# Kernel optimization log

Measured on AMD Instinct MI355X. Metric: run time of the kernel, lower is better.

The kernel has to match this reference:

```python
import jax, jax.numpy as jnp
import numpy as np

VAR0, VAR1 = 0.1, 0.2
THRESHOLD = 0.35
NEGPOS_RATIO = 7
LOW_GT_THRESH = 0.2  # match() filters GT whose best prior IoU < 0.2


def setup_inputs() -> dict:
    key = jax.random.key(0)
    ks = jax.random.split(key, 8)
    B, P, G = 16, 43008, 128
    loc_data = jax.random.normal(ks[0], (B, P, 4), jnp.float32)
    conf_data = jax.random.normal(ks[1], (B, P, 2), jnp.float32)
    landm_data = jax.random.normal(ks[2], (B, P, 10), jnp.float32)
    # priors in cxcywh form, positive sizes
    pc = jax.random.uniform(ks[3], (P, 2), jnp.float32)
    pwh = jax.random.uniform(ks[4], (P, 2), jnp.float32, minval=0.02, maxval=0.32)
    priors = jnp.concatenate([pc, pwh], axis=1)
    # targets: valid xyxy boxes + 10 landmark coords + label (face=1)
    ctr = jax.random.uniform(ks[5], (B, G, 2), jnp.float32, minval=0.2, maxval=0.8)
    wh = jax.random.uniform(ks[6], (B, G, 2), jnp.float32, minval=0.05, maxval=0.3)
    boxes = jnp.concatenate([ctr - wh / 2, ctr + wh / 2], axis=-1)
    landms = jax.random.uniform(ks[7], (B, G, 10), jnp.float32)
    labels = jnp.ones((B, G, 1), jnp.float32)
    targets = jnp.concatenate([boxes, landms, labels], axis=-1)
    return {"loc_data": loc_data, "conf_data": conf_data, "landm_data": landm_data,
            "priors": priors, "targets": targets}


def point_form(priors):
    return jnp.concatenate([priors[:, :2] - priors[:, 2:] / 2,
                            priors[:, :2] + priors[:, 2:] / 2], axis=1)


def jaccard(a, b):  # a: [G,4] xyxy, b: [P,4] xyxy -> [G,P]
    lt = jnp.maximum(a[:, None, :2], b[None, :, :2])
    rb = jnp.minimum(a[:, None, 2:], b[None, :, 2:])
    wh = jnp.clip(rb - lt, 0.0)
    inter = wh[..., 0] * wh[..., 1]
    area_a = (a[:, 2] - a[:, 0]) * (a[:, 3] - a[:, 1])
    area_b = (b[:, 2] - b[:, 0]) * (b[:, 3] - b[:, 1])
    return inter / (area_a[:, None] + area_b[None, :] - inter)


def encode(matched, priors):  # matched xyxy [P,4], priors cxcywh [P,4]
    g_cxcy = (matched[:, :2] + matched[:, 2:]) / 2 - priors[:, :2]
    g_cxcy = g_cxcy / (VAR0 * priors[:, 2:])
    g_wh = jnp.log((matched[:, 2:] - matched[:, :2]) / priors[:, 2:]) / VAR1
    return jnp.concatenate([g_cxcy, g_wh], axis=1)


def encode_landm(matched, priors):  # matched [P,10], priors [P,4]
    m = matched.reshape(-1, 5, 2)
    g = (m - priors[:, None, :2]) / (VAR0 * priors[:, None, 2:])
    return g.reshape(-1, 10)


def match_one(truths, labels, landms, priors):
    G = truths.shape[0]
    overlaps = jaccard(truths, point_form(priors))  # [G, P]
    best_prior_overlap = overlaps.max(axis=1)       # [G]
    best_prior_idx = overlaps.argmax(axis=1)        # [G]
    valid = best_prior_overlap >= LOW_GT_THRESH
    any_valid = jnp.any(valid)
    best_truth_overlap = overlaps.max(axis=0)       # [P]
    best_truth_idx = overlaps.argmax(axis=0)        # [P]
    # index_fill_(0, best_prior_idx_filter, 2): ensure each valid GT keeps its best prior
    fill_val = jnp.where(valid, 2.0, best_truth_overlap[best_prior_idx])
    best_truth_overlap = best_truth_overlap.at[best_prior_idx].set(fill_val)
    # best_truth_idx[best_prior_idx[j]] = j for all j
    best_truth_idx = best_truth_idx.at[best_prior_idx].set(jnp.arange(G))
    matches = truths[best_truth_idx]                       # [P,4]
    conf = labels[best_truth_idx].astype(jnp.int32)        # [P]
    conf = jnp.where(best_truth_overlap < THRESHOLD, 0, conf)
    conf = jnp.where(any_valid, conf, 0)  # no valid GT -> all background
    loc = encode(matches, priors)
    landm = encode_landm(landms[best_truth_idx], priors)
    return loc, conf, landm


def smooth_l1(x):
    ax = jnp.abs(x)
    return jnp.where(ax < 1.0, 0.5 * ax * ax, ax - 0.5)


def reference(loc_data, conf_data, landm_data, priors, targets):
    truths = targets[..., :4]
    landms = targets[..., 4:14]
    labels = targets[..., 14]
    loc_t, conf_t, landm_t = jax.vmap(
        lambda t, l, lm: match_one(t, l, lm, priors))(truths, labels, landms)

    # landmark loss over positives
    pos1 = conf_t > 0
    N1 = jnp.maximum(pos1.sum().astype(jnp.float32), 1.0)
    loss_landm = jnp.sum(smooth_l1(landm_data - landm_t) * pos1[..., None])

    # localization loss over positives
    pos = conf_t != 0
    num_pos = pos.sum(axis=1, keepdims=True)  # [B,1]
    loss_l = jnp.sum(smooth_l1(loc_data - loc_t) * pos[..., None])

    # hard negative mining on per-prior CE loss
    lse = jax.scipy.special.logsumexp(conf_data, axis=-1)  # [B,P]
    gathered = jnp.take_along_axis(conf_data, conf_t[..., None], axis=-1)[..., 0]
    ce_all = lse - gathered                                # [B,P] per-prior CE
    mine = jnp.where(pos, 0.0, ce_all)
    loss_idx = jnp.argsort(-mine, axis=1)
    idx_rank = jnp.argsort(loss_idx, axis=1)
    num_neg = jnp.clip(NEGPOS_RATIO * num_pos, None, pos.shape[1] - 1)
    neg = idx_rank < num_neg
    sel = pos | neg
    loss_c = jnp.sum(jnp.where(sel, ce_all, 0.0))

    N = jnp.maximum(num_pos.sum().astype(jnp.float32), 1.0)
    return loss_l / N, loss_c / N, loss_landm / N1
```

## Files before the change

### kernel.cpp

```cpp
#include <hip/hip_runtime.h>
#include <stdint.h>


#define GC 8
#define PPI 2
#define NCELL 1024

__device__ __forceinline__ float sl1(float x) {
  float a = fabsf(x);
  return a < 1.f ? 0.5f * a * a : a - 0.5f;
}

__device__ __forceinline__ double dwave(double v) {
#pragma unroll
  for (int o = 32; o; o >>= 1) v += __shfl_down(v, o);
  return v;
}

__device__ __forceinline__ int cellOf(float4 pr) {
  int cx = (int)(pr.x * 16.f); cx = cx < 0 ? 0 : (cx > 15 ? 15 : cx);
  int cy = (int)(pr.y * 16.f); cy = cy < 0 ? 0 : (cy > 15 ? 15 : cy);
  return ((cy * 16 + cx) << 2) | ((pr.z > 0.17f) ? 2 : 0) |
         ((pr.w > 0.17f) ? 1 : 0);
}

__device__ __forceinline__ unsigned bsufscan(unsigned x, unsigned* S,
                                             unsigned* wt, int tid) {
  int lane = tid & 63, wid = tid >> 6;
  unsigned v = x;
#pragma unroll
  for (int o = 1; o < 64; o <<= 1) {
    unsigned u = __shfl_down(v, o);
    if (lane + o < 64) v += u;
  }
  if (lane == 0) wt[wid] = v;
  __syncthreads();
  if (wid == 0) {
    unsigned tv = (lane < 16) ? wt[lane] : 0;
#pragma unroll
    for (int o = 1; o < 16; o <<= 1) {
      unsigned u = __shfl_down(tv, o);
      if (lane + o < 64) tv += u;
    }
    if (lane < 16) wt[lane] = tv;
  }
  __syncthreads();
  unsigned Sv = v + ((wid < 15) ? wt[wid + 1] : 0u);
  S[tid] = Sv;
  __syncthreads();
  return Sv;
}

__global__ __launch_bounds__(256) void k_hist(const float* __restrict__ priors,
                                              unsigned* __restrict__ cellh,
                                              int P) {
  int p = blockIdx.x * 256 + threadIdx.x;
  if (p < P) {
    float4 pr = ((const float4*)priors)[p];
    atomicAdd(&cellh[cellOf(pr)], 1u);
  }
}

__global__ __launch_bounds__(1024) void k_scan(const unsigned* __restrict__ cellh,
                                               unsigned* __restrict__ cellcur) {
  int tid = threadIdx.x;
  __shared__ unsigned s[NCELL];
  unsigned v = cellh[tid];
  s[tid] = v;
  __syncthreads();
  for (int off = 1; off < NCELL; off <<= 1) {
    unsigned a = (tid >= off) ? s[tid - off] : 0u;
    __syncthreads();
    s[tid] += a;
    __syncthreads();
  }
  cellcur[tid] = s[tid] - v;
}

__global__ __launch_bounds__(256) void k_scatter(
    const float* __restrict__ priors, unsigned* __restrict__ cellcur,
    float4* __restrict__ spr, unsigned* __restrict__ sid,
    unsigned* __restrict__ inv, int P) {
  int p = blockIdx.x * 256 + threadIdx.x;
  if (p < P) {
    float4 pr = ((const float4*)priors)[p];
    unsigned pos = atomicAdd(&cellcur[cellOf(pr)], 1u);
    spr[pos] = pr;
    sid[pos] = (unsigned)p;
    inv[p] = pos;
  }
}

__global__ __launch_bounds__(64) void k_wgm(
    const float4* __restrict__ spr, const float* __restrict__ targets,
    uint4* __restrict__ gmask, unsigned* __restrict__ zbase, int zwords,
    int G, int NRW, int B, int P) {
  int run = blockIdx.x, lane = threadIdx.x;
  for (int i = run * 64 + lane; i < zwords; i += NRW * 64) zbase[i] = 0u;

  int p = run * 64 + lane;
  float x1 = 1e30f, y1 = 1e30f, x2 = -1e30f, y2 = -1e30f;
  if (p < P) {
    float4 pr = spr[p];
    x1 = pr.x - pr.z * 0.5f; y1 = pr.y - pr.w * 0.5f;
    x2 = pr.x + pr.z * 0.5f; y2 = pr.y + pr.w * 0.5f;
  }
#pragma unroll
  for (int o = 32; o; o >>= 1) {
    x1 = fminf(x1, __shfl_down(x1, o));
    y1 = fminf(y1, __shfl_down(y1, o));
    x2 = fmaxf(x2, __shfl_down(x2, o));
    y2 = fmaxf(y2, __shfl_down(y2, o));
  }
  x1 = __shfl(x1, 0); y1 = __shfl(y1, 0);
  x2 = __shfl(x2, 0); y2 = __shfl(y2, 0);

  for (int b = 0; b < B; ++b) {
    const float* t0 = targets + ((size_t)b * G + lane) * 15;
    const float* t1 = targets + ((size_t)b * G + lane + 64) * 15;
    bool o0 = (t0[0] < x2) && (x1 < t0[2]) && (t0[1] < y2) && (y1 < t0[3]);
    bool o1 = (t1[0] < x2) && (x1 < t1[2]) && (t1[1] < y2) && (y1 < t1[3]);
    unsigned long long b0 = __ballot(o0);
    unsigned long long b1 = __ballot(o1);
    if (lane == 0)
      gmask[(size_t)b * NRW + run] =
          make_uint4((unsigned)b0, (unsigned)(b0 >> 32), (unsigned)b1,
                     (unsigned)(b1 >> 32));
  }
}

__global__ __launch_bounds__(256) void k_mm(
    const float4* __restrict__ spr, const unsigned* __restrict__ sid,
    const uint4* __restrict__ gmask, const float* __restrict__ conf,
    const float* __restrict__ targets, const float* __restrict__ loc,
    const float* __restrict__ lm, uint2* __restrict__ ovti,
    unsigned long long* __restrict__ bp, float* __restrict__ mine,
    unsigned* __restrict__ ghist, double* __restrict__ pll,
    double* __restrict__ pllm, double* __restrict__ plc,
    double* __restrict__ msum, int* __restrict__ pnp, int P, int G, int NIOU,
    int PTI, int NGC, int PC, int NRW) {
  int tid = threadIdx.x;
  __shared__ char smem[16384];
  __shared__ float4 sgt[128];
  __shared__ float sga[128];

  if ((int)blockIdx.x < NIOU) {
    float* st = (float*)smem;
    double* rs = (double*)(smem + 7680);
    int* ri = (int*)(smem + 7808);
    unsigned* hist = (unsigned*)(smem + 8192);
    unsigned* smaskw = (unsigned*)(smem + 12288);
    int b = blockIdx.x / PTI, tile = blockIdx.x % PTI;
    int base = tile * (256 * PPI);
    for (int i = tid; i < G * 15; i += 256)
      st[i] = targets[(size_t)b * G * 15 + i];
    for (int g = tid; g < G; g += 256) {
      const float* t = targets + ((size_t)b * G + g) * 15;
      float x1 = t[0], y1 = t[1], x2 = t[2], y2 = t[3];
      sgt[g] = make_float4(x1, y1, x2, y2);
      sga[g] = (x2 - x1) * (y2 - y1);
    }
    for (int i = tid; i < 1024; i += 256) hist[i] = 0;
    if (tid < 8 * 4)
      smaskw[tid] =
          ((const unsigned*)(gmask + (size_t)b * NRW + tile * (4 * PPI)))[tid];
    __syncthreads();

    float px1[PPI], py1[PPI], px2[PPI], py2[PPI], pa[PPI];
    float bi[PPI], sb[PPI];
    int bidx[PPI];
#pragma unroll
    for (int k = 0; k < PPI; ++k) {
      int p = base + tid + k * 256;
      int pl = p < P ? p : P - 1;
      float4 pr = spr[pl];
      px1[k] = pr.x - pr.z * 0.5f; py1[k] = pr.y - pr.w * 0.5f;
      px2[k] = pr.x + pr.z * 0.5f; py2[k] = pr.y + pr.w * 0.5f;
      pa[k] = pr.z * pr.w;
      bi[k] = 0.f; sb[k] = 1.f; bidx[k] = 0;
    }

#define IOU_UPD(GG)                                                        \
  {                                                                        \
    float iw = fminf(T.z, px2[k]) - fmaxf(T.x, px1[k]);                    \
    float ih = fminf(T.w, py2[k]) - fmaxf(T.y, py1[k]);                    \
    float inter = fmaxf(iw, 0.f) * ih;                                     \
    float S = A + pa[k];                                                   \
    if (inter * sb[k] > bi[k] * S) { bi[k] = inter; sb[k] = S; bidx[k] = (GG); } \
  }
#pragma unroll
    for (int k = 0; k < PPI; ++k) {
      int runl = k * 4 + (tid >> 6);
      unsigned mw0 = smaskw[runl * 4 + 0], mw1 = smaskw[runl * 4 + 1];
      unsigned mw2 = smaskw[runl * 4 + 2], mw3 = smaskw[runl * 4 + 3];
      unsigned long long m0 =
          ((unsigned long long)(unsigned)__builtin_amdgcn_readfirstlane(
               (int)mw1)
           << 32) |
          (unsigned)__builtin_amdgcn_readfirstlane((int)mw0);
      unsigned long long m1 =
          ((unsigned long long)(unsigned)__builtin_amdgcn_readfirstlane(
               (int)mw3)
           << 32) |
          (unsigned)__builtin_amdgcn_readfirstlane((int)mw2);
      while (m0) {
        int g = __builtin_ctzll(m0);
        m0 &= m0 - 1;
        float4 T = sgt[g];
        float A = sga[g];
        IOU_UPD(g)
      }
      while (m1) {
        int g = 64 + __builtin_ctzll(m1);
        m1 &= m1 - 1;
        float4 T = sgt[g];
        float A = sga[g];
        IOU_UPD(g)
      }
    }
#undef IOU_UPD

    double ll = 0, llm = 0, lc = 0, ms = 0;
    int np = 0;
#pragma unroll
    for (int k = 0; k < PPI; ++k) {
      int p = base + tid + k * 256;
      if (p < P) {
        size_t idxs = (size_t)b * P + p;
        float ov = bi[k] / (sb[k] - bi[k]);
        int ti = bidx[k];
        ovti[idxs] = make_uint2(__float_as_uint(ov), (unsigned)ti);
        bool pos = ov >= 0.35f;
        unsigned op = sid[p];
        size_t idxo = (size_t)b * P + op;
        float2 c = ((const float2*)conf)[idxo];
        float mx = fmaxf(c.x, c.y);
        float dd = fabsf(c.x - c.y);
        float lse = mx + logf(1.f + expf(-dd));
        float ce = lse - (pos ? c.y : c.x);
        float mv = pos ? 0.f : ce;
        mine[idxs] = mv;
        atomicAdd(&hist[__float_as_uint(mv) >> 21], 1u);
        ms += (double)mv;
        if (pos) {
          np++;
          lc += (double)ce;
          float4 pr = spr[p];
          const float* t = st + ti * 15;
          float rz = 1.f / pr.z, rw = 1.f / pr.w;
          float rdx = 10.f * rz, rdy = 10.f * rw;
          float gx = ((t[0] + t[2]) * 0.5f - pr.x) * rdx;
          float gy = ((t[1] + t[3]) * 0.5f - pr.y) * rdy;
          float gw = logf((t[2] - t[0]) * rz) * 5.0f;
          float gh = logf((t[3] - t[1]) * rw) * 5.0f;
          float4 ld = ((const float4*)loc)[idxo];
          ll += (double)(sl1(ld.x - gx) + sl1(ld.y - gy) + sl1(ld.z - gw) +
                         sl1(ld.w - gh));
          const float2* lmd = (const float2*)lm + idxo * 5;
          float s = 0.f;
#pragma unroll
          for (int j = 0; j < 5; ++j) {
            float2 lv = lmd[j];
            float ex = (t[4 + 2 * j] - pr.x) * rdx;
            float ey = (t[5 + 2 * j] - pr.y) * rdy;
            s += sl1(lv.x - ex) + sl1(lv.y - ey);
          }
          llm += (double)s;
        }
      }
    }

    ll = dwave(ll); llm = dwave(llm); lc = dwave(lc); ms = dwave(ms);
#pragma unroll
    for (int o = 32; o; o >>= 1) np += __shfl_down(np, o);
    int lane = tid & 63, wid = tid >> 6;
    if (lane == 0) {
      rs[wid] = ll; rs[4 + wid] = llm; rs[8 + wid] = lc; rs[12 + wid] = ms;
      ri[wid] = np;
    }
    __syncthreads();
    if (tid == 0) {
      pll[blockIdx.x] = rs[0] + rs[1] + rs[2] + rs[3];
      pllm[blockIdx.x] = rs[4] + rs[5] + rs[6] + rs[7];
      plc[blockIdx.x] = rs[8] + rs[9] + rs[10] + rs[11];
      msum[blockIdx.x] = rs[12] + rs[13] + rs[14] + rs[15];
      pnp[blockIdx.x] = ri[0] + ri[1] + ri[2] + ri[3];
    }
    for (int i = tid; i < 1024; i += 256) {
      unsigned c = hist[i];
      if (c) atomicAdd(&ghist[b * 1024 + i], c);
    }
  } else {
    unsigned long long* sred = (unsigned long long*)smem;
    unsigned char* bm = (unsigned char*)sga;
    int bc = blockIdx.x - NIOU;
    int pc = bc % PC;
    int gcb = (bc / PC) % NGC;
    int b = bc / (PC * NGC);
    int g0 = gcb * GC;

    int chunk = (P + PC - 1) / PC;
    int ps = pc * chunk;
    int pe = ps + chunk; if (pe > P) pe = P;
    int count = pe - ps;
    int nrun = (count + 63) >> 6;

    if (tid < GC) {
      int g = g0 + tid;
      float4 v = make_float4(0.f, 0.f, 0.f, 0.f);
      if (g < G) {
        const float* t = targets + ((size_t)b * G + g) * 15;
        v = make_float4(t[0], t[1], t[2], t[3]);
      }
      sgt[tid] = v;
    }
    if (tid < nrun) {
      uint4 m = gmask[(size_t)b * NRW + (ps >> 6) + tid];
      unsigned word = (g0 & 64) ? ((g0 & 32) ? m.w : m.z)
                                : ((g0 & 32) ? m.y : m.x);
      bm[tid] = (unsigned char)((word >> (g0 & 31)) & 0xffu);
    }
    __syncthreads();

    float gx1[GC], gy1[GC], gx2[GC], gy2[GC], ga[GC];
#pragma unroll
    for (int j = 0; j < GC; ++j) {
      float4 T = sgt[j];
      gx1[j] = T.x; gy1[j] = T.y; gx2[j] = T.z; gy2[j] = T.w;
      ga[j] = (T.z - T.x) * (T.w - T.y);
    }

    float bi[GC], sb[GC];
    unsigned bpp[GC];
#pragma unroll
    for (int j = 0; j < GC; ++j) { bi[j] = 0.f; sb[j] = 1.f; bpp[j] = 0xFFFFFFFFu; }

#define BP_BODY(X1, Y1, X2, Y2, AR, PP)                                     \
  {                                                                         \
    float iw = fminf(gx2[j], X2) - fmaxf(gx1[j], X1);                       \
    float ih = fminf(gy2[j], Y2) - fmaxf(gy1[j], Y1);                       \
    float inter = fmaxf(iw, 0.f) * ih;                                      \
    float S = ga[j] + AR;                                                   \
    if (inter * sb[j] > bi[j] * S) { bi[j] = inter; sb[j] = S; bpp[j] = (PP); } \
  }
    for (int i = tid; i < count; i += 1024) {
      int ib = __builtin_amdgcn_readfirstlane(i);
      int rl = ib >> 6;
      int i1 = i + 256, i2 = i + 512, i3 = i + 768;
      int p0 = ps + i;
      int p1 = (i1 < count) ? ps + i1 : p0;
      int p2 = (i2 < count) ? ps + i2 : p0;
      int p3 = (i3 < count) ? ps + i3 : p0;
      unsigned by0 = bm[rl];
      unsigned by1 = bm[(ib + 256 < count) ? rl + 4 : rl];
      unsigned by2 = bm[(ib + 512 < count) ? rl + 8 : rl];
      unsigned by3 = bm[(ib + 768 < count) ? rl + 12 : rl];
      by0 = (unsigned)__builtin_amdgcn_readfirstlane((int)by0);
      by1 = (unsigned)__builtin_amdgcn_readfirstlane((int)by1);
      by2 = (unsigned)__builtin_amdgcn_readfirstlane((int)by2);
      by3 = (unsigned)__builtin_amdgcn_readfirstlane((int)by3);
      float4 q0 = spr[p0];
      float4 q1 = spr[p1];
      float4 q2 = spr[p2];
      float4 q3 = spr[p3];
      unsigned s0 = sid[p0], s1 = sid[p1], s2 = sid[p2], s3 = sid[p3];
      float ax1 = q0.x - q0.z * 0.5f, ay1 = q0.y - q0.w * 0.5f;
      float ax2 = q0.x + q0.z * 0.5f, ay2 = q0.y + q0.w * 0.5f;
      float aa = q0.z * q0.w;
      float bx1 = q1.x - q1.z * 0.5f, by1f = q1.y - q1.w * 0.5f;
      float bx2 = q1.x + q1.z * 0.5f, by2f = q1.y + q1.w * 0.5f;
      float ba = q1.z * q1.w;
      float cx1 = q2.x - q2.z * 0.5f, cy1 = q2.y - q2.w * 0.5f;
      float cx2 = q2.x + q2.z * 0.5f, cy2 = q2.y + q2.w * 0.5f;
      float ca = q2.z * q2.w;
      float dx1 = q3.x - q3.z * 0.5f, dy1 = q3.y - q3.w * 0.5f;
      float dx2 = q3.x + q3.z * 0.5f, dy2 = q3.y + q3.w * 0.5f;
      float da = q3.z * q3.w;
#pragma unroll
      for (int j = 0; j < GC; ++j) {
        if (by0 & (1u << j)) BP_BODY(ax1, ay1, ax2, ay2, aa, s0)
        if (by1 & (1u << j)) BP_BODY(bx1, by1f, bx2, by2f, ba, s1)
        if (by2 & (1u << j)) BP_BODY(cx1, cy1, cx2, cy2, ca, s2)
        if (by3 & (1u << j)) BP_BODY(dx1, dy1, dx2, dy2, da, s3)
      }
    }
#undef BP_BODY

#pragma unroll
    for (int j = 0; j < GC; ++j) {
      float iou = bi[j] / (sb[j] - bi[j]);
      unsigned long long pk =
          ((unsigned long long)__float_as_uint(iou) << 32) | (unsigned)(~bpp[j]);
      sred[j * 256 + tid] = pk;
    }
    __syncthreads();
    {
      int j = tid >> 5, s = tid & 31;
      unsigned long long m = sred[j * 256 + s];
#pragma unroll
      for (int t = 1; t < 8; ++t) {
        unsigned long long v = sred[j * 256 + s + t * 32];
        if (v > m) m = v;
      }
      __syncthreads();
      sred[j * 256 + s] = m;
    }
    __syncthreads();
    if (tid < GC) {
      unsigned long long m = sred[tid * 256];
      for (int s = 1; s < 32; ++s) {
        unsigned long long v = sred[tid * 256 + s];
        if (v > m) m = v;
      }
      int g = g0 + tid;
      if (g < G) atomicMax(&bp[(size_t)b * G + g], m);
    }
  }
}

__global__ __launch_bounds__(1024) void k_tail2(
    const unsigned long long* __restrict__ bp, const unsigned* __restrict__ inv,
    uint2* __restrict__ ovti, const float* __restrict__ conf,
    const float* __restrict__ loc, const float* __restrict__ lm,
    const float* __restrict__ priors, const float* __restrict__ targets,
    float* __restrict__ mine, unsigned* __restrict__ ghist,
    const int* __restrict__ pnp, const double* __restrict__ msum,
    const double* __restrict__ pll, const double* __restrict__ pllm,
    const double* __restrict__ plc, double* __restrict__ gacc,
    int* __restrict__ gnp, unsigned* __restrict__ done,
    float* __restrict__ out, int P, int G, int PTI, int B) {
  int b = blockIdx.x, tid = threadIdx.x;
  int lane = tid & 63, wid = tid >> 6;
  __shared__ unsigned spp[128];
  __shared__ double rs[16 * 5];
  __shared__ int ris[16];
  __shared__ unsigned S[1024];
  __shared__ unsigned hs[2048];
  __shared__ unsigned wt[16];
  __shared__ double sdel[4];
  __shared__ int sdnp, sav, smode;
  __shared__ long long sk;
  __shared__ double sA, sC, sD;
  __shared__ int snpos;
  __shared__ int st_, sk1_;
  __shared__ unsigned lcnt;
  __shared__ int spf21, sk2;
  __shared__ unsigned stb;
  __shared__ double stie;

  double dll = 0, dllm = 0, dlc = 0, dms = 0;
  int dnp = 0;
  unsigned pp = 0;
  bool valid = false;
  if (tid < G) {
    unsigned long long m = bp[(size_t)b * G + tid];
    pp = (m == 0ull) ? 0u : ~(unsigned)m;
    float val = __uint_as_float((unsigned)(m >> 32));
    spp[tid] = pp;
    valid = val >= 0.2f;
  }
  int av = __syncthreads_or((tid < G && valid) ? 1 : 0);
  bool win = false;
  if (tid < G) {
    win = true;
    for (int g2 = tid + 1; g2 < G; ++g2)
      if (spp[g2] == pp) { win = false; break; }
  }
  if (win) {
    size_t idx = (size_t)b * P + pp;
    unsigned sp = inv[pp];
    size_t idxs = (size_t)b * P + sp;
    uint2 ot = ovti[idxs];
    float ov_o = __uint_as_float(ot.x);
    int ti_o = (int)ot.y;
    float ov_n = valid ? 2.0f : ov_o;
    int ti_n = tid;
    bool pos_o = ov_o >= 0.35f, pos_n = ov_n >= 0.35f;

    float2 c = ((const float2*)conf)[idx];
    float mx = fmaxf(c.x, c.y);
    float dd = fabsf(c.x - c.y);
    float lse = mx + logf(1.f + expf(-dd));
    float ce_o = lse - (pos_o ? c.y : c.x);
    float ce_n = lse - (pos_n ? c.y : c.x);
    float mv_o = mine[idxs];
    float mv_n = pos_n ? 0.f : ce_n;
    if (mv_n != mv_o) {
      mine[idxs] = mv_n;
      atomicSub(&ghist[b * 1024 + (__float_as_uint(mv_o) >> 21)], 1u);
      atomicAdd(&ghist[b * 1024 + (__float_as_uint(mv_n) >> 21)], 1u);
    }
    dms = (double)mv_n - (double)mv_o;
    dnp = (pos_n ? 1 : 0) - (pos_o ? 1 : 0);
    dlc = (pos_n ? (double)ce_n : 0.0) - (pos_o ? (double)ce_o : 0.0);

    if (pos_o || pos_n) {
      float4 pr = ((const float4*)priors)[pp];
      float rz = 1.f / pr.z, rw = 1.f / pr.w;
      float rdx = 10.f * rz, rdy = 10.f * rw;
      float4 ld = ((const float4*)loc)[idx];
      const float2* lmd = (const float2*)lm + idx * 5;
      float2 lv[5];
#pragma unroll
      for (int j = 0; j < 5; ++j) lv[j] = lmd[j];
      for (int pass = 0; pass < 2; ++pass) {
        bool act = pass ? pos_n : pos_o;
        int ti = pass ? ti_n : ti_o;
        if (!act) continue;
        const float* t = targets + ((size_t)b * G + ti) * 15;
        float gx = ((t[0] + t[2]) * 0.5f - pr.x) * rdx;
        float gy = ((t[1] + t[3]) * 0.5f - pr.y) * rdy;
        float gw = logf((t[2] - t[0]) * rz) * 5.0f;
        float gh = logf((t[3] - t[1]) * rw) * 5.0f;
        double l = (double)(sl1(ld.x - gx) + sl1(ld.y - gy) +
                            sl1(ld.z - gw) + sl1(ld.w - gh));
        float s = 0.f;
#pragma unroll
        for (int j = 0; j < 5; ++j) {
          float ex = (t[4 + 2 * j] - pr.x) * rdx;
          float ey = (t[5 + 2 * j] - pr.y) * rdy;
          s += sl1(lv[j].x - ex) + sl1(lv[j].y - ey);
        }
        if (pass) { dll += l; dllm += (double)s; }
        else { dll -= l; dllm -= (double)s; }
      }
    }
  }
  dll = dwave(dll); dllm = dwave(dllm); dlc = dwave(dlc); dms = dwave(dms);
#pragma unroll
  for (int o = 32; o; o >>= 1) dnp += __shfl_down(dnp, o);
  if (lane == 0) {
    rs[wid] = dll; rs[16 + wid] = dllm; rs[32 + wid] = dlc; rs[48 + wid] = dms;
    ris[wid] = dnp;
  }
  __syncthreads();
  if (tid == 0) {
    double a = 0, c2 = 0, d2 = 0, m2 = 0;
    int n2 = 0;
    for (int i = 0; i < 16; ++i) {
      a += rs[i]; c2 += rs[16 + i]; d2 += rs[32 + i]; m2 += rs[48 + i];
      n2 += ris[i];
    }
    sdel[0] = a; sdel[1] = c2; sdel[2] = d2; sdel[3] = m2;
    sdnp = n2; sav = av;
  }
  __syncthreads();

  double a = 0, cc = 0, d = 0, ms = 0;
  int n = 0;
  for (int i = tid; i < PTI; i += 1024) {
    int ix = b * PTI + i;
    a += pll[ix]; cc += pllm[ix]; d += plc[ix]; ms += msum[ix]; n += pnp[ix];
  }
  a = dwave(a); cc = dwave(cc); d = dwave(d); ms = dwave(ms);
#pragma unroll
  for (int o = 32; o; o >>= 1) n += __shfl_down(n, o);
  if (lane == 0) {
    rs[wid] = a; rs[16 + wid] = cc; rs[32 + wid] = d; rs[48 + wid] = ms;
    ris[wid] = n;
  }
  __syncthreads();
  double Fv = 0.0;
  if (tid == 0) {
    double A = 0, C = 0, D = 0, MS = 0;
    int npos = 0;
    for (int i = 0; i < 16; ++i) {
      A += rs[i]; C += rs[16 + i]; D += rs[32 + i]; MS += rs[48 + i];
      npos += ris[i];
    }
    A += sdel[0]; C += sdel[1]; D += sdel[2]; MS += sdel[3];
    npos += sdnp;
    if (!sav) { A = 0; C = 0; D = 0; npos = 0; }
    sA = A; sC = C; sD = D; snpos = npos;
    long long k = 7LL * (long long)npos;
    long long cap = P - 1;
    int md = 1;
    if (k <= 0) { Fv = 0.0; md = 0; }
    else if (k >= cap) { Fv = MS; md = 0; }
    smode = md; sk = k;
  }
  __syncthreads();

  if (smode) {
    long long k = sk;
    {
      unsigned x = ghist[b * 1024 + tid];
      unsigned Sv = bsufscan(x, S, wt, tid);
      int cnt_ = __syncthreads_count((long long)Sv >= k);
      int seg = cnt_ - 1;
      if (tid == seg) {
        long long cum = (seg + 1 < 1024) ? (long long)S[seg + 1] : 0;
        st_ = seg;
        sk1_ = (int)(k - cum);
      }
      if (tid == 0) lcnt = 0;
    }
    __syncthreads();
    int t = st_;
    long long k1 = (long long)sk1_;

    const float* mrow = mine + (size_t)b * P;
    float* crow = (float*)(ovti + (size_t)b * P);
    double acc = 0;
    for (int base0 = 0; base0 < P; base0 += 4096) {
#pragma unroll
      for (int j = 0; j < 4; ++j) {
        int p = base0 + tid + j * 1024;
        bool keep = false;
        unsigned bb = 0;
        if (p < P) {
          bb = __float_as_uint(mrow[p]);
          int bin = (int)(bb >> 21);
          if (bin > t) acc += (double)__uint_as_float(bb);
          else keep = (bin == t);
        }
        unsigned long long mk = __ballot(keep);
        int nset = __popcll(mk);
        if (nset) {
          unsigned wbase = 0;
          if (lane == 0) wbase = atomicAdd(&lcnt, (unsigned)nset);
          wbase = __shfl(wbase, 0);
          if (keep) {
            int offi = __popcll(mk & ((1ull << lane) - 1ull));
            crow[wbase + offi] = __uint_as_float(bb);
          }
        }
      }
    }
    acc = dwave(acc);
    if (lane == 0) rs[wid] = acc;
    __syncthreads();
    int nn = (int)lcnt;

    hs[tid] = 0; hs[tid + 1024] = 0;
    __syncthreads();
    for (int i = tid; i < nn; i += 1024) {
      unsigned bb = __float_as_uint(crow[i]);
      atomicAdd(&hs[(bb >> 10) & 2047], 1u);
    }
    __syncthreads();
    {
      unsigned h0 = hs[tid * 2], h1v = hs[tid * 2 + 1];
      unsigned Sv = bsufscan(h0 + h1v, S, wt, tid);
      int cnt_ = __syncthreads_count((long long)Sv >= k1);
      int seg = cnt_ - 1;
      if (tid == seg) {
        long long cum = (seg + 1 < 1024) ? (long long)S[seg + 1] : 0;
        int bin = seg * 2;
        if (cum + h1v >= k1) bin = seg * 2 + 1;
        else cum += h1v;
        spf21 = (t << 11) | bin;
        sk2 = (int)(k1 - cum);
      }
    }
    __syncthreads();
    int pf21 = spf21;

    hs[tid] = 0;
    __syncthreads();
    for (int i = tid; i < nn; i += 1024) {
      unsigned bb = __float_as_uint(crow[i]);
      if ((int)(bb >> 10) == pf21) atomicAdd(&hs[bb & 1023], 1u);
    }
    __syncthreads();
    {
      unsigned Sv = bsufscan(hs[tid], S, wt, tid);
      long long kk = (long long)sk2;
      int cnt_ = __syncthreads_count((long long)Sv >= kk);
      int seg = cnt_ - 1;
      if (tid == seg) {
        long long cum = (seg + 1 < 1024) ? (long long)S[seg + 1] : 0;
        unsigned tb = ((unsigned)pf21 << 10) | (unsigned)seg;
        stb = tb;
        stie = (double)(kk - cum) * (double)__uint_as_float(tb);
      }
    }
    __syncthreads();

    unsigned tb = stb;
    double v = 0.0;
    for (int i = tid; i < nn; i += 1024) {
      unsigned bb = __float_as_uint(crow[i]);
      if (bb > tb) v += (double)__uint_as_float(bb);
    }
    v = dwave(v);
    if (lane == 0) rs[16 + wid] = v;
    __syncthreads();
    if (tid == 0) {
      double hi = 0, vt = 0;
      for (int i = 0; i < 16; ++i) { hi += rs[i]; vt += rs[16 + i]; }
      Fv = hi + vt + stie;
    }
  }

  if (tid == 0) {
    atomicAdd(&gacc[0], sA);
    atomicAdd(&gacc[1], sC);
    atomicAdd(&gacc[2], sD);
    atomicAdd(&gacc[3], Fv);
    atomicAdd(gnp, snpos);
    __threadfence();
    unsigned old = atomicAdd(done, 1u);
    if (old == (unsigned)B - 1) {
      __threadfence();
      double A = atomicAdd(&gacc[0], 0.0);
      double C = atomicAdd(&gacc[1], 0.0);
      double D = atomicAdd(&gacc[2], 0.0);
      double F = atomicAdd(&gacc[3], 0.0);
      int N = atomicAdd(gnp, 0);
      double Nd = N < 1 ? 1.0 : (double)N;
      out[0] = (float)(A / Nd);
      out[1] = (float)((D + F) / Nd);
      out[2] = (float)(C / Nd);
    }
  }
}

extern "C" void kernel_launch(void* const* d_in, const int* in_sizes, int n_in,
                              void* d_out, int out_size, void* d_ws,
                              size_t ws_size, hipStream_t stream) {
  const float* loc = (const float*)d_in[0];
  const float* conf = (const float*)d_in[1];
  const float* lm = (const float*)d_in[2];
  const float* priors = (const float*)d_in[3];
  const float* targets = (const float*)d_in[4];

  int P = in_sizes[3] / 4;
  int B = in_sizes[0] / (4 * P);
  int G = in_sizes[4] / (15 * B);
  int PTI = (P + 256 * PPI - 1) / (256 * PPI);
  int NIOU = B * PTI;
  int NGC = (G + GC - 1) / GC;
  int PC = 8;
  int NBP = B * NGC * PC;
  int NPB = (P + 255) / 256;
  int NRW = (P + 63) / 64;
  int NW = B * NRW;

  char* w = (char*)d_ws;
  size_t off = 0;
  unsigned long long* bp = (unsigned long long*)(w + off);
  off += (size_t)B * G * 8;
  unsigned* ghist = (unsigned*)(w + off);
  off += (size_t)B * 1024 * 4;
  double* gacc = (double*)(w + off);
  off += 4 * 8;
  int* gnp = (int*)(w + off);
  off += 4;
  unsigned* done = (unsigned*)(w + off);
  off += 4;
  size_t clear_bytes = off;
  off = (off + 255) & ~(size_t)255;
  float4* spr = (float4*)(w + off);
  off += (size_t)NRW * 64 * 16;
  unsigned* sid = (unsigned*)(w + off);
  off += (size_t)P * 4;
  unsigned* inv = (unsigned*)(w + off);
  off += (size_t)P * 4;
  uint4* gmask = (uint4*)(w + off);
  off += (size_t)NW * 16;
  unsigned* cellh = (unsigned*)(w + off);
  off += (size_t)NCELL * 4;
  unsigned* cellcur = (unsigned*)(w + off);
  off += (size_t)NCELL * 4;
  off = (off + 255) & ~(size_t)255;
  uint2* ovti = (uint2*)(w + off);
  off += (size_t)B * P * 8;
  float* mine = (float*)(w + off);
  off += (size_t)B * P * 4;
  double* pll = (double*)(w + off);
  off += (size_t)NIOU * 8;
  double* pllm = (double*)(w + off);
  off += (size_t)NIOU * 8;
  double* plc = (double*)(w + off);
  off += (size_t)NIOU * 8;
  double* msum = (double*)(w + off);
  off += (size_t)NIOU * 8;
  int* pnp = (int*)(w + off);
  off += (size_t)NIOU * 4;

  hipMemsetAsync(cellh, 0, (size_t)NCELL * 4, stream);

  k_hist<<<NPB, 256, 0, stream>>>(priors, cellh, P);
  k_scan<<<1, 1024, 0, stream>>>(cellh, cellcur);
  k_scatter<<<NPB, 256, 0, stream>>>(priors, cellcur, spr, sid, inv, P);
  k_wgm<<<NRW, 64, 0, stream>>>(spr, targets, gmask, (unsigned*)w,
                                (int)(clear_bytes / 4), G, NRW, B, P);
  k_mm<<<NIOU + NBP, 256, 0, stream>>>(spr, sid, gmask, conf, targets, loc,
                                       lm, ovti, bp, mine, ghist, pll, pllm,
                                       plc, msum, pnp, P, G, NIOU, PTI, NGC,
                                       PC, NRW);
  k_tail2<<<B, 1024, 0, stream>>>(bp, inv, ovti, conf, loc, lm, priors,
                                  targets, mine, ghist, pnp, msum, pll, pllm,
                                  plc, gacc, gnp, done, (float*)d_out, P, G,
                                  PTI, B);
}
```

Measured before the change: 202.5 us.

## Fuse prior sort prep into one cooperative kernel and raise PPI to four

Replaces the memset plus four small launches (histogram, scan, scatter, window-mask) with one cooperative kernel that uses grid-wide syncs between phases. The per-block scan is rewritten with wave shuffles. PPI is doubled so each IoU block handles more priors, and the mask-load count is adjusted to match. Grid syncs have their own cost, and NPB blocks (168) must all be co-resident for the cooperative launch to succeed. Fewer IoU blocks may also lower parallelism in k_mm.

```diff
diff --git a/kernel.cpp b/kernel.cpp
--- a/kernel.cpp
+++ b/kernel.cpp
@@ -1,9 +1,12 @@
 #include <hip/hip_runtime.h>
+#include <hip/hip_cooperative_groups.h>
 #include <stdint.h>
 
+namespace cg = cooperative_groups;
+
 
 #define GC 8
-#define PPI 2
+#define PPI 4
 #define NCELL 1024
 
 __device__ __forceinline__ float sl1(float x) {
@@ -51,81 +54,92 @@
   return Sv;
 }
 
-__global__ __launch_bounds__(256) void k_hist(const float* __restrict__ priors,
-                                              unsigned* __restrict__ cellh,
-                                              int P) {
-  int p = blockIdx.x * 256 + threadIdx.x;
-  if (p < P) {
-    float4 pr = ((const float4*)priors)[p];
+__global__ __launch_bounds__(256) void k_prep(
+    const float* __restrict__ priors, const float* __restrict__ targets,
+    float4* __restrict__ spr, unsigned* __restrict__ sid,
+    unsigned* __restrict__ inv, uint4* __restrict__ gmask,
+    unsigned* __restrict__ cellh, unsigned* __restrict__ cellcur,
+    unsigned* __restrict__ zbase, int zwords, int P, int G, int NRW, int B) {
+  cg::grid_group grid = cg::this_grid();
+  __shared__ unsigned wsum[4];
+  int tid = threadIdx.x;
+  int gid = blockIdx.x * 256 + tid;
+  int total = gridDim.x * 256;
+
+  for (int i = gid; i < zwords; i += total) zbase[i] = 0u;
+  for (int i = gid; i < NCELL; i += total) cellh[i] = 0u;
+  grid.sync();
+
+  if (gid < P) {
+    float4 pr = ((const float4*)priors)[gid];
     atomicAdd(&cellh[cellOf(pr)], 1u);
   }
-}
-
-__global__ __launch_bounds__(1024) void k_scan(const unsigned* __restrict__ cellh,
-                                               unsigned* __restrict__ cellcur) {
-  int tid = threadIdx.x;
-  __shared__ unsigned s[NCELL];
-  unsigned v = cellh[tid];
-  s[tid] = v;
-  __syncthreads();
-  for (int off = 1; off < NCELL; off <<= 1) {
-    unsigned a = (tid >= off) ? s[tid - off] : 0u;
-    __syncthreads();
-    s[tid] += a;
-    __syncthreads();
-  }
-  cellcur[tid] = s[tid] - v;
-}
-
-__global__ __launch_bounds__(256) void k_scatter(
-    const float* __restrict__ priors, unsigned* __restrict__ cellcur,
-    float4* __restrict__ spr, unsigned* __restrict__ sid,
-    unsigned* __restrict__ inv, int P) {
-  int p = blockIdx.x * 256 + threadIdx.x;
-  if (p < P) {
-    float4 pr = ((const float4*)priors)[p];
+  grid.sync();
+
+  if (blockIdx.x == 0) {
+    int lane = tid & 63, wv = tid >> 6;
+    unsigned v0 = cellh[tid * 4 + 0], v1 = cellh[tid * 4 + 1];
+    unsigned v2 = cellh[tid * 4 + 2], v3 = cellh[tid * 4 + 3];
+    unsigned tot = v0 + v1 + v2 + v3;
+    unsigned x = tot;
+#pragma unroll
+    for (int o = 1; o < 64; o <<= 1) {
+      unsigned u = __shfl_up(x, o);
+      if (lane >= o) x += u;
+    }
+    if (lane == 63) wsum[wv] = x;
+    __syncthreads();
+    unsigned base = 0;
+    for (int j = 0; j < wv; ++j) base += wsum[j];
+    unsigned exc = base + x - tot;
+    cellcur[tid * 4 + 0] = exc;
+    cellcur[tid * 4 + 1] = exc + v0;
+    cellcur[tid * 4 + 2] = exc + v0 + v1;
+    cellcur[tid * 4 + 3] = exc + v0 + v1 + v2;
+  }
+  grid.sync();
+
+  if (gid < P) {
+    float4 pr = ((const float4*)priors)[gid];
     unsigned pos = atomicAdd(&cellcur[cellOf(pr)], 1u);
     spr[pos] = pr;
-    sid[pos] = (unsigned)p;
-    inv[p] = pos;
-  }
-}
-
-__global__ __launch_bounds__(64) void k_wgm(
-    const float4* __restrict__ spr, const float* __restrict__ targets,
-    uint4* __restrict__ gmask, unsigned* __restrict__ zbase, int zwords,
-    int G, int NRW, int B, int P) {
-  int run = blockIdx.x, lane = threadIdx.x;
-  for (int i = run * 64 + lane; i < zwords; i += NRW * 64) zbase[i] = 0u;
-
-  int p = run * 64 + lane;
-  float x1 = 1e30f, y1 = 1e30f, x2 = -1e30f, y2 = -1e30f;
-  if (p < P) {
-    float4 pr = spr[p];
-    x1 = pr.x - pr.z * 0.5f; y1 = pr.y - pr.w * 0.5f;
-    x2 = pr.x + pr.z * 0.5f; y2 = pr.y + pr.w * 0.5f;
-  }
-#pragma unroll
-  for (int o = 32; o; o >>= 1) {
-    x1 = fminf(x1, __shfl_down(x1, o));
-    y1 = fminf(y1, __shfl_down(y1, o));
-    x2 = fmaxf(x2, __shfl_down(x2, o));
-    y2 = fmaxf(y2, __shfl_down(y2, o));
-  }
-  x1 = __shfl(x1, 0); y1 = __shfl(y1, 0);
-  x2 = __shfl(x2, 0); y2 = __shfl(y2, 0);
-
-  for (int b = 0; b < B; ++b) {
-    const float* t0 = targets + ((size_t)b * G + lane) * 15;
-    const float* t1 = targets + ((size_t)b * G + lane + 64) * 15;
-    bool o0 = (t0[0] < x2) && (x1 < t0[2]) && (t0[1] < y2) && (y1 < t0[3]);
-    bool o1 = (t1[0] < x2) && (x1 < t1[2]) && (t1[1] < y2) && (y1 < t1[3]);
-    unsigned long long b0 = __ballot(o0);
-    unsigned long long b1 = __ballot(o1);
-    if (lane == 0)
-      gmask[(size_t)b * NRW + run] =
-          make_uint4((unsigned)b0, (unsigned)(b0 >> 32), (unsigned)b1,
-                     (unsigned)(b1 >> 32));
+    sid[pos] = (unsigned)gid;
+    inv[gid] = pos;
+  }
+  grid.sync();
+
+  {
+    int wv = tid >> 6, lane = tid & 63;
+    for (int run = blockIdx.x * 4 + wv; run < NRW; run += gridDim.x * 4) {
+      int p = run * 64 + lane;
+      float x1 = 1e30f, y1 = 1e30f, x2 = -1e30f, y2 = -1e30f;
+      if (p < P) {
+        float4 pr = spr[p];
+        x1 = pr.x - pr.z * 0.5f; y1 = pr.y - pr.w * 0.5f;
+        x2 = pr.x + pr.z * 0.5f; y2 = pr.y + pr.w * 0.5f;
+      }
+#pragma unroll
+      for (int o = 32; o; o >>= 1) {
+        x1 = fminf(x1, __shfl_down(x1, o));
+        y1 = fminf(y1, __shfl_down(y1, o));
+        x2 = fmaxf(x2, __shfl_down(x2, o));
+        y2 = fmaxf(y2, __shfl_down(y2, o));
+      }
+      x1 = __shfl(x1, 0); y1 = __shfl(y1, 0);
+      x2 = __shfl(x2, 0); y2 = __shfl(y2, 0);
+      for (int b = 0; b < B; ++b) {
+        const float* t0 = targets + ((size_t)b * G + lane) * 15;
+        const float* t1 = targets + ((size_t)b * G + lane + 64) * 15;
+        bool o0 = (t0[0] < x2) && (x1 < t0[2]) && (t0[1] < y2) && (y1 < t0[3]);
+        bool o1 = (t1[0] < x2) && (x1 < t1[2]) && (t1[1] < y2) && (y1 < t1[3]);
+        unsigned long long b0 = __ballot(o0);
+        unsigned long long b1 = __ballot(o1);
+        if (lane == 0)
+          gmask[(size_t)b * NRW + run] =
+              make_uint4((unsigned)b0, (unsigned)(b0 >> 32), (unsigned)b1,
+                         (unsigned)(b1 >> 32));
+      }
+    }
   }
 }
 
@@ -161,7 +175,7 @@
       sga[g] = (x2 - x1) * (y2 - y1);
     }
     for (int i = tid; i < 1024; i += 256) hist[i] = 0;
-    if (tid < 8 * 4)
+    if (tid < 4 * PPI * 4)
       smaskw[tid] =
           ((const unsigned*)(gmask + (size_t)b * NRW + tile * (4 * PPI)))[tid];
     __syncthreads();
@@ -779,13 +793,16 @@
   int* pnp = (int*)(w + off);
   off += (size_t)NIOU * 4;
 
-  hipMemsetAsync(cellh, 0, (size_t)NCELL * 4, stream);
-
-  k_hist<<<NPB, 256, 0, stream>>>(priors, cellh, P);
-  k_scan<<<1, 1024, 0, stream>>>(cellh, cellcur);
-  k_scatter<<<NPB, 256, 0, stream>>>(priors, cellcur, spr, sid, inv, P);
-  k_wgm<<<NRW, 64, 0, stream>>>(spr, targets, gmask, (unsigned*)w,
-                                (int)(clear_bytes / 4), G, NRW, B, P);
+  unsigned* zbase = (unsigned*)w;
+  int zwords = (int)(clear_bytes / 4);
+
+  void* pargs[] = {(void*)&priors, (void*)&targets, (void*)&spr, (void*)&sid,
+                   (void*)&inv,    (void*)&gmask,   (void*)&cellh,
+                   (void*)&cellcur, (void*)&zbase,  (void*)&zwords,
+                   (void*)&P,      (void*)&G,       (void*)&NRW, (void*)&B};
+  hipLaunchCooperativeKernel((void*)k_prep, dim3(NPB), dim3(256), pargs, 0,
+                             stream);
+
   k_mm<<<NIOU + NBP, 256, 0, stream>>>(spr, sid, gmask, conf, targets, loc,
                                        lm, ovti, bp, mine, ghist, pll, pllm,
                                        plc, msum, pnp, P, G, NIOU, PTI, NGC,
```

Result: slower. 283.6 us (+40.0%).
